# Kernel optimization log

Hardware: AMD Instinct MI355X
Metric: run time of the kernel (lower is better)

Reference implementation:

```python
import jax, jax.numpy as jnp
import numpy as np

N = 500_000      # nodes
B = 8192         # graphs
F = 128          # num_node_features
C = 128          # channels (num_out_features)
EPS = 1e-16      # matches torch_geometric.utils.softmax denominator eps


def setup_inputs() -> dict:
    key = jax.random.key(0)
    ks = jax.random.split(key, 16)
    w = lambda k, shape: jax.random.normal(k, shape, dtype=jnp.float32) * 0.02
    inp = {
        "x": jax.random.normal(ks[0], (N, F), dtype=jnp.float32),
        "u": jax.random.normal(ks[1], (B, C), dtype=jnp.float32),
        "batch": jnp.sort(jax.random.randint(ks[2], (N,), 0, B, dtype=jnp.int32)),
        "size": B,
        # gate_nn: Linear(C,C) -> ReLU -> Linear(C,1)
        "gate_w1": w(ks[3], (C, C)), "gate_b1": w(ks[4], (C,)),
        "gate_w2": w(ks[5], (C, 1)), "gate_b2": w(ks[6], (1,)),
        # node_nn: Linear(F,C) -> ReLU -> Linear(C,C)
        "node_w1": w(ks[7], (F, C)), "node_b1": w(ks[8], (C,)),
        "node_w2": w(ks[9], (C, C)), "node_b2": w(ks[10], (C,)),
        # ques_nn: Linear(C,C) -> ReLU -> Linear(C,C)
        "ques_w1": w(ks[11], (C, C)), "ques_b1": w(ks[12], (C,)),
        "ques_w2": w(ks[13], (C, C)), "ques_b2": w(ks[14], (C,)),
    }
    return inp


def _mlp2(x, w1, b1, w2, b2):
    return jax.nn.relu(x @ w1 + b1) @ w2 + b2


def reference(x, u, batch, size,
              gate_w1, gate_b1, gate_w2, gate_b2,
              node_w1, node_b1, node_w2, node_b2,
              ques_w1, ques_b1, ques_w2, ques_b2):
    # node features h_theta(x): [N, C]
    h = _mlp2(x, node_w1, node_b1, node_w2, node_b2)
    # question features per graph, gathered to nodes: [N, C]
    q = _mlp2(u, ques_w1, ques_b1, ques_w2, ques_b2)
    # gate scores: [N, 1]
    gate = _mlp2(q[batch] * h, gate_w1, gate_b1, gate_w2, gate_b2)
    # segment softmax over graphs (torch_geometric.utils.softmax)
    m = jax.ops.segment_max(gate, batch, num_segments=size)          # [B, 1]
    m = jnp.where(jnp.isfinite(m), m, 0.0)                            # empty segments
    e = jnp.exp(gate - m[batch])                                      # [N, 1]
    s = jax.ops.segment_sum(e, batch, num_segments=size)              # [B, 1]
    alpha = e / (s[batch] + EPS)                                      # [N, 1]
    # scatter_add pooling: [B, C]
    out = jax.ops.segment_sum(alpha * h, batch, num_segments=size)
    return out
```

## Files before the change

### kernel.cpp

```cpp
#include <hip/hip_runtime.h>
#include <math.h>

#define NN 500000
#define NB 8192
#define GMAX 16
#define HG_GRID 1536
#define HG_NT ((NN + 63) / 64)

typedef _Float16 f16x8 __attribute__((ext_vector_type(8)));
typedef __fp16 fp16x2 __attribute__((ext_vector_type(2)));
typedef float f32x4 __attribute__((ext_vector_type(4)));

__device__ inline f16x8 cvt8(float4 a, float4 b) {
    union { fp16x2 p[4]; f16x8 r; } u;
    u.p[0] = __builtin_amdgcn_cvt_pkrtz(a.x, a.y);
    u.p[1] = __builtin_amdgcn_cvt_pkrtz(a.z, a.w);
    u.p[2] = __builtin_amdgcn_cvt_pkrtz(b.x, b.y);
    u.p[3] = __builtin_amdgcn_cvt_pkrtz(b.z, b.w);
    return u.r;
}

__global__ void prep_w(const float* __restrict__ nw1, const float* __restrict__ nw2,
                       const float* __restrict__ gw1, const float* __restrict__ gw2,
                       const float* __restrict__ qw1, const float* __restrict__ qw2,
                       _Float16* __restrict__ wT1, _Float16* __restrict__ wT2,
                       _Float16* __restrict__ wTg, _Float16* __restrict__ wTq1,
                       _Float16* __restrict__ wTq2, _Float16* __restrict__ g2h) {
    int k = blockIdx.x;
    int n = threadIdx.x;
    wT1[n * 128 + k]  = (_Float16)nw1[k * 128 + n];
    wT2[n * 128 + k]  = (_Float16)nw2[k * 128 + n];
    wTg[n * 128 + k]  = (_Float16)gw1[k * 128 + n];
    wTq1[n * 128 + k] = (_Float16)qw1[k * 128 + n];
    wTq2[n * 128 + k] = (_Float16)qw2[k * 128 + n];
    if (k == 0) g2h[n] = (_Float16)gw2[n];
}

__launch_bounds__(512, 4)
__global__ void q_kernel(const float* __restrict__ u,
                         const _Float16* __restrict__ wTq1, const _Float16* __restrict__ wTq2,
                         const float* __restrict__ qb1, const float* __restrict__ qb2,
                         _Float16* __restrict__ q, float* __restrict__ Ppre, float* __restrict__ s) {
    __shared__ __align__(16) _Float16 tbuf[128][136];
    const int tid  = threadIdx.x;
    const int wave = tid >> 6;
    const int lane = tid & 63;
    const int lrow = lane & 15;
    const int quad = lane >> 4;
    const int wr   = wave >> 1;
    const int wc   = wave & 1;
    const int row0 = blockIdx.x * 128;
    const int rbase = wr * 32;

    for (int idx = tid; idx < 128 * 128; idx += 512) Ppre[(size_t)row0 * 128 + idx] = 0.f;
    if (tid < 128) s[row0 + tid] = 0.f;

    f32x4 acc[2][4];
    const f32x4 fz = {0.f, 0.f, 0.f, 0.f};
#pragma unroll
    for (int mi = 0; mi < 2; ++mi)
#pragma unroll
        for (int ci = 0; ci < 4; ++ci) acc[mi][ci] = fz;

#pragma unroll
    for (int ki = 0; ki < 4; ++ki) {
        const int k = ki * 32 + quad * 8;
        f16x8 a[2];
#pragma unroll
        for (int mi = 0; mi < 2; ++mi) {
            int r = row0 + rbase + mi * 16 + lrow;
            const float4* up = (const float4*)(u + (size_t)r * 128 + k);
            a[mi] = cvt8(up[0], up[1]);
        }
        f16x8 b[4];
#pragma unroll
        for (int ci = 0; ci < 4; ++ci)
            b[ci] = *(const f16x8*)(wTq1 + (size_t)(wc * 64 + ci * 16 + lrow) * 128 + k);
#pragma unroll
        for (int mi = 0; mi < 2; ++mi)
#pragma unroll
            for (int ci = 0; ci < 4; ++ci)
                acc[mi][ci] = __builtin_amdgcn_mfma_f32_16x16x32_f16(a[mi], b[ci], acc[mi][ci], 0, 0, 0);
    }
#pragma unroll
    for (int ci = 0; ci < 4; ++ci) {
        int c = wc * 64 + ci * 16 + lrow;
        float bv = qb1[c];
#pragma unroll
        for (int mi = 0; mi < 2; ++mi)
#pragma unroll
            for (int i = 0; i < 4; ++i) {
                int r = rbase + mi * 16 + quad * 4 + i;
                tbuf[r][c] = (_Float16)fmaxf(acc[mi][ci][i] + bv, 0.f);
            }
    }
    __syncthreads();

#pragma unroll
    for (int mi = 0; mi < 2; ++mi)
#pragma unroll
        for (int ci = 0; ci < 4; ++ci) acc[mi][ci] = fz;
#pragma unroll
    for (int ki = 0; ki < 4; ++ki) {
        const int k = ki * 32 + quad * 8;
        f16x8 a[2];
#pragma unroll
        for (int mi = 0; mi < 2; ++mi)
            a[mi] = *(const f16x8*)&tbuf[rbase + mi * 16 + lrow][k];
        f16x8 b[4];
#pragma unroll
        for (int ci = 0; ci < 4; ++ci)
            b[ci] = *(const f16x8*)(wTq2 + (size_t)(wc * 64 + ci * 16 + lrow) * 128 + k);
#pragma unroll
        for (int mi = 0; mi < 2; ++mi)
#pragma unroll
            for (int ci = 0; ci < 4; ++ci)
                acc[mi][ci] = __builtin_amdgcn_mfma_f32_16x16x32_f16(a[mi], b[ci], acc[mi][ci], 0, 0, 0);
    }
#pragma unroll
    for (int ci = 0; ci < 4; ++ci) {
        int c = wc * 64 + ci * 16 + lrow;
        float bv = qb2[c];
#pragma unroll
        for (int mi = 0; mi < 2; ++mi)
#pragma unroll
            for (int i = 0; i < 4; ++i) {
                int r = row0 + rbase + mi * 16 + quad * 4 + i;
                q[(size_t)r * 128 + c] = (_Float16)(acc[mi][ci][i] + bv);
            }
    }
}

__launch_bounds__(256, 1)
__global__ void hg_kernel(const float* __restrict__ x, const int* __restrict__ batch,
                          const _Float16* __restrict__ qglob,
                          const _Float16* __restrict__ wT1, const _Float16* __restrict__ wT2,
                          const _Float16* __restrict__ wTg, const _Float16* __restrict__ g2h,
                          const float* __restrict__ nb1, const float* __restrict__ nb2,
                          const float* __restrict__ gb1, const float* __restrict__ gb2,
                          float* __restrict__ Ppre, float* __restrict__ s) {
    __shared__ __align__(16) _Float16 t1buf[2][64][136];
    __shared__ __align__(16) _Float16 Ebuf[2][GMAX][136];
    __shared__ __align__(16) _Float16 scratch[64][136];

    const int tid  = threadIdx.x;
    const int wave = tid >> 6;
    const int lane = tid & 63;
    const int lrow = lane & 15;
    const int quad = lane >> 4;
    const int rbase = wave * 16;
    const int blk  = (int)blockIdx.x;
    const f32x4 fz = {0.f, 0.f, 0.f, 0.f};

    f16x8 a16[4];
    {
        int r = min(blk * 64 + rbase + lrow, NN - 1);
        const float4* xp = (const float4*)(x + (size_t)r * 128 + quad * 8);
#pragma unroll
        for (int ki = 0; ki < 4; ++ki)
            a16[ki] = cvt8(xp[ki * 8], xp[ki * 8 + 1]);
    }
    int bv = batch[min(blk * 64 + lane, NN - 1)];

    int pb = 0;
    for (int t = blk; t < HG_NT; t += HG_GRID, pb ^= 1) {
        const int row0  = t * 64;
        const int rown0 = (t + HG_GRID) * 64;

        const int b_lo = __shfl(bv, 0, 64);
        int rel = bv - b_lo;
#pragma unroll
        for (int off = 32; off >= 1; off >>= 1) rel = max(rel, __shfl_xor(rel, off, 64));
        const int gcnt = min(rel + 1, GMAX);
        int gown[4];
#pragma unroll
        for (int i = 0; i < 4; ++i)
            gown[i] = __shfl(bv, rbase + quad * 4 + i, 64) - b_lo;
        int bv_next = batch[min(rown0 + lane, NN - 1)];

        {
            int g  = lane >> 2;
            int rr = (lane & 3) * 4;
            *(float2*)&Ebuf[pb][g][rbase + rr] = make_float2(0.f, 0.f);
        }

        f32x4 acc[8];
#pragma unroll
        for (int ci = 0; ci < 8; ++ci) acc[ci] = fz;
#pragma unroll
        for (int ki = 0; ki < 4; ++ki) {
            const int k = ki * 32 + quad * 8;
            f16x8 b[8];
#pragma unroll
            for (int ci = 0; ci < 8; ++ci)
                b[ci] = *(const f16x8*)(wT1 + (size_t)(ci * 16 + lrow) * 128 + k);
#pragma unroll
            for (int ci = 0; ci < 8; ++ci)
                acc[ci] = __builtin_amdgcn_mfma_f32_16x16x32_f16(a16[ki], b[ci], acc[ci], 0, 0, 0);
        }
#pragma unroll
        for (int ci = 0; ci < 8; ++ci) {
            int c = ci * 16 + lrow;
            float bv1 = nb1[c];
#pragma unroll
            for (int i = 0; i < 4; ++i)
                t1buf[pb][rbase + quad * 4 + i][c] = (_Float16)fmaxf(acc[ci][i] + bv1, 0.f);
        }

        __builtin_amdgcn_sched_barrier(0);
        float4 xraw[4][2];
        {
            int r = min(rown0 + rbase + lrow, NN - 1);
            const float4* xp = (const float4*)(x + (size_t)r * 128 + quad * 8);
#pragma unroll
            for (int ki = 0; ki < 4; ++ki) {
                xraw[ki][0] = xp[ki * 8];
                xraw[ki][1] = xp[ki * 8 + 1];
            }
        }

#pragma unroll
        for (int ci = 0; ci < 8; ++ci) acc[ci] = fz;
#pragma unroll
        for (int ki = 0; ki < 4; ++ki) {
            const int k = ki * 32 + quad * 8;
            f16x8 a = *(const f16x8*)&t1buf[pb][rbase + lrow][k];
            f16x8 b[8];
#pragma unroll
            for (int ci = 0; ci < 8; ++ci)
                b[ci] = *(const f16x8*)(wT2 + (size_t)(ci * 16 + lrow) * 128 + k);
#pragma unroll
            for (int ci = 0; ci < 8; ++ci)
                acc[ci] = __builtin_amdgcn_mfma_f32_16x16x32_f16(a, b[ci], acc[ci], 0, 0, 0);
        }
        {
            float nb2c[8];
#pragma unroll
            for (int ci = 0; ci < 8; ++ci) nb2c[ci] = nb2[ci * 16 + lrow];
#pragma unroll
            for (int i = 0; i < 4; ++i) {
                const _Float16* qrow = qglob + (size_t)(b_lo + gown[i]) * 128;
                int r = rbase + quad * 4 + i;
#pragma unroll
                for (int ci = 0; ci < 8; ++ci) {
                    int c = ci * 16 + lrow;
                    float h = acc[ci][i] + nb2c[ci];
                    scratch[r][c] = (_Float16)((float)qrow[c] * h);
                }
            }
        }

#pragma unroll
        for (int ci = 0; ci < 8; ++ci) acc[ci] = fz;
#pragma unroll
        for (int ki = 0; ki < 4; ++ki) {
            const int k = ki * 32 + quad * 8;
            f16x8 a = *(const f16x8*)&scratch[rbase + lrow][k];
            f16x8 b[8];
#pragma unroll
            for (int ci = 0; ci < 8; ++ci)
                b[ci] = *(const f16x8*)(wTg + (size_t)(ci * 16 + lrow) * 128 + k);
#pragma unroll
            for (int ci = 0; ci < 8; ++ci)
                acc[ci] = __builtin_amdgcn_mfma_f32_16x16x32_f16(a, b[ci], acc[ci], 0, 0, 0);
        }
        {
            float p[4] = {0.f, 0.f, 0.f, 0.f};
#pragma unroll
            for (int ci = 0; ci < 8; ++ci) {
                int c = ci * 16 + lrow;
                float b1 = gb1[c];
                float w = (float)g2h[c];
#pragma unroll
                for (int i = 0; i < 4; ++i)
                    p[i] = fmaf(fmaxf(acc[ci][i] + b1, 0.f), w, p[i]);
            }
#pragma unroll
            for (int off = 1; off <= 8; off <<= 1)
#pragma unroll
                for (int i = 0; i < 4; ++i)
                    p[i] += __shfl_xor(p[i], off, 64);
            const float gb2v = gb2[0];
            if (lrow == 0) {
#pragma unroll
                for (int i = 0; i < 4; ++i) {
                    int r = rbase + quad * 4 + i;
                    bool valid = (row0 + r) < NN;
                    float e = valid ? __expf(p[i] + gb2v) : 0.f;
                    int g = gown[i];
                    if (g < GMAX) {
                        Ebuf[pb][g][r] = (_Float16)e;
                    } else if (valid) {
                        atomicAdd(&s[b_lo + g], e);
                        for (int c = 0; c < 128; ++c)
                            atomicAdd(&Ppre[(size_t)(b_lo + g) * 128 + c],
                                      e * (float)t1buf[pb][r][c]);
                    }
                }
            }
        }

#pragma unroll
        for (int ki = 0; ki < 4; ++ki)
            a16[ki] = cvt8(xraw[ki][0], xraw[ki][1]);
        bv = bv_next;

        __syncthreads();

        f16x8 aE[2];
#pragma unroll
        for (int ki2 = 0; ki2 < 2; ++ki2)
            aE[ki2] = *(const f16x8*)&Ebuf[pb][lrow][ki2 * 32 + quad * 8];
        f32x4 pacc[2] = {fz, fz};
#pragma unroll
        for (int ci2 = 0; ci2 < 2; ++ci2) {
            int col = wave * 32 + ci2 * 16 + lrow;
#pragma unroll
            for (int ki2 = 0; ki2 < 2; ++ki2) {
                f16x8 bh;
#pragma unroll
                for (int j = 0; j < 8; ++j) bh[j] = t1buf[pb][ki2 * 32 + quad * 8 + j][col];
                pacc[ci2] = __builtin_amdgcn_mfma_f32_16x16x32_f16(aE[ki2], bh, pacc[ci2], 0, 0, 0);
            }
        }
#pragma unroll
        for (int ci2 = 0; ci2 < 2; ++ci2)
#pragma unroll
            for (int i = 0; i < 4; ++i) {
                int g = quad * 4 + i;
                if (g < gcnt)
                    atomicAdd(&Ppre[(size_t)(b_lo + g) * 128 + wave * 32 + ci2 * 16 + lrow],
                              pacc[ci2][i]);
            }
        if (wave == 0) {
            float sv = 0.f;
#pragma unroll
            for (int j = 0; j < 16; ++j) sv += (float)Ebuf[pb][lrow][quad * 16 + j];
            sv += __shfl_xor(sv, 16, 64);
            sv += __shfl_xor(sv, 32, 64);
            if (quad == 0 && lrow < gcnt) atomicAdd(&s[b_lo + lrow], sv);
        }
    }
}

__launch_bounds__(512, 4)
__global__ void fin_kernel(const float* __restrict__ Ppre, const float* __restrict__ s,
                           const _Float16* __restrict__ wT2, const float* __restrict__ nb2,
                           float* __restrict__ out) {
    const int tid  = threadIdx.x;
    const int wave = tid >> 6;
    const int lane = tid & 63;
    const int lrow = lane & 15;
    const int quad = lane >> 4;
    const int wr   = wave >> 1;
    const int wc   = wave & 1;
    const int row0 = blockIdx.x * 128;
    const int rbase = wr * 32;

    f32x4 acc[2][4];
    const f32x4 fz = {0.f, 0.f, 0.f, 0.f};
#pragma unroll
    for (int mi = 0; mi < 2; ++mi)
#pragma unroll
        for (int ci = 0; ci < 4; ++ci) acc[mi][ci] = fz;
#pragma unroll
    for (int ki = 0; ki < 4; ++ki) {
        const int k = ki * 32 + quad * 8;
        f16x8 a[2];
#pragma unroll
        for (int mi = 0; mi < 2; ++mi) {
            int r = row0 + rbase + mi * 16 + lrow;
            const float4* pp = (const float4*)(Ppre + (size_t)r * 128 + k);
            a[mi] = cvt8(pp[0], pp[1]);
        }
        f16x8 b[4];
#pragma unroll
        for (int ci = 0; ci < 4; ++ci)
            b[ci] = *(const f16x8*)(wT2 + (size_t)(wc * 64 + ci * 16 + lrow) * 128 + k);
#pragma unroll
        for (int mi = 0; mi < 2; ++mi)
#pragma unroll
            for (int ci = 0; ci < 4; ++ci)
                acc[mi][ci] = __builtin_amdgcn_mfma_f32_16x16x32_f16(a[mi], b[ci], acc[mi][ci], 0, 0, 0);
    }
    float sv[2][4], rinv[2][4];
#pragma unroll
    for (int mi = 0; mi < 2; ++mi)
#pragma unroll
        for (int i = 0; i < 4; ++i) {
            int r = row0 + rbase + mi * 16 + quad * 4 + i;
            sv[mi][i] = s[r];
            rinv[mi][i] = 1.f / (sv[mi][i] + 1e-16f);
        }
#pragma unroll
    for (int ci = 0; ci < 4; ++ci) {
        int c = wc * 64 + ci * 16 + lrow;
        float bv = nb2[c];
#pragma unroll
        for (int mi = 0; mi < 2; ++mi)
#pragma unroll
            for (int i = 0; i < 4; ++i) {
                int r = row0 + rbase + mi * 16 + quad * 4 + i;
                out[(size_t)r * 128 + c] = (acc[mi][ci][i] + sv[mi][i] * bv) * rinv[mi][i];
            }
    }
}

extern "C" void kernel_launch(void* const* d_in, const int* in_sizes, int n_in,
                              void* d_out, int out_size, void* d_ws, size_t ws_size,
                              hipStream_t stream) {
    const float* x    = (const float*)d_in[0];
    const float* u    = (const float*)d_in[1];
    const int* batch  = (const int*)d_in[2];
    const float* gw1  = (const float*)d_in[4];
    const float* gb1  = (const float*)d_in[5];
    const float* gw2  = (const float*)d_in[6];
    const float* gb2  = (const float*)d_in[7];
    const float* nw1  = (const float*)d_in[8];
    const float* nb1  = (const float*)d_in[9];
    const float* nw2  = (const float*)d_in[10];
    const float* nb2  = (const float*)d_in[11];
    const float* qw1  = (const float*)d_in[12];
    const float* qb1  = (const float*)d_in[13];
    const float* qw2  = (const float*)d_in[14];
    const float* qb2  = (const float*)d_in[15];

    char* ws = (char*)d_ws;
    _Float16* q   = (_Float16*)ws;
    float* Ppre   = (float*)(ws + 2097152);
    float* s      = (float*)(ws + 6291456);
    _Float16* wT1 = (_Float16*)(ws + 6324224);
    _Float16* wT2  = wT1 + 16384;
    _Float16* wTg  = wT2 + 16384;
    _Float16* wTq1 = wTg + 16384;
    _Float16* wTq2 = wTq1 + 16384;
    _Float16* g2h  = wTq2 + 16384;
    float* out = (float*)d_out;

    hipLaunchKernelGGL(prep_w, dim3(128), dim3(128), 0, stream,
                       nw1, nw2, gw1, gw2, qw1, qw2, wT1, wT2, wTg, wTq1, wTq2, g2h);
    hipLaunchKernelGGL(q_kernel, dim3(NB / 128), dim3(512), 0, stream,
                       u, wTq1, wTq2, qb1, qb2, q, Ppre, s);
    hipLaunchKernelGGL(hg_kernel, dim3(HG_GRID), dim3(256), 0, stream,
                       x, batch, q, wT1, wT2, wTg, g2h, nb1, nb2, gb1, gb2, Ppre, s);
    hipLaunchKernelGGL(fin_kernel, dim3(NB / 128), dim3(512), 0, stream,
                       Ppre, s, wT2, nb2, out);
}
```

Baseline: 598.4 us.

## Double hg_kernel row tile to 128 per block and split next-tile x prefetch

Result: faster. 563.3 us (-5.9%).

```diff
diff --git a/kernel.cpp b/kernel.cpp
--- a/kernel.cpp
+++ b/kernel.cpp
@@ -4,8 +4,9 @@
 #define NN 500000
 #define NB 8192
 #define GMAX 16
-#define HG_GRID 1536
-#define HG_NT ((NN + 63) / 64)
+#define TROWS 128
+#define HG_GRID 512
+#define HG_NT ((NN + TROWS - 1) / TROWS)
 
 typedef _Float16 f16x8 __attribute__((ext_vector_type(8)));
 typedef __fp16 fp16x2 __attribute__((ext_vector_type(2)));
@@ -36,12 +37,12 @@
     if (k == 0) g2h[n] = (_Float16)gw2[n];
 }
 
-__launch_bounds__(512, 4)
+__launch_bounds__(256, 2)
 __global__ void q_kernel(const float* __restrict__ u,
                          const _Float16* __restrict__ wTq1, const _Float16* __restrict__ wTq2,
                          const float* __restrict__ qb1, const float* __restrict__ qb2,
                          _Float16* __restrict__ q, float* __restrict__ Ppre, float* __restrict__ s) {
-    __shared__ __align__(16) _Float16 tbuf[128][136];
+    __shared__ __align__(16) _Float16 tbuf[64][136];
     const int tid  = threadIdx.x;
     const int wave = tid >> 6;
     const int lane = tid & 63;
@@ -49,11 +50,11 @@
     const int quad = lane >> 4;
     const int wr   = wave >> 1;
     const int wc   = wave & 1;
-    const int row0 = blockIdx.x * 128;
+    const int row0 = (int)blockIdx.x * 64;
     const int rbase = wr * 32;
 
-    for (int idx = tid; idx < 128 * 128; idx += 512) Ppre[(size_t)row0 * 128 + idx] = 0.f;
-    if (tid < 128) s[row0 + tid] = 0.f;
+    for (int idx = tid; idx < 64 * 128; idx += 256) Ppre[(size_t)row0 * 128 + idx] = 0.f;
+    if (tid < 64) s[row0 + tid] = 0.f;
 
     f32x4 acc[2][4];
     const f32x4 fz = {0.f, 0.f, 0.f, 0.f};
@@ -139,54 +140,62 @@
                           const float* __restrict__ nb1, const float* __restrict__ nb2,
                           const float* __restrict__ gb1, const float* __restrict__ gb2,
                           float* __restrict__ Ppre, float* __restrict__ s) {
-    __shared__ __align__(16) _Float16 t1buf[2][64][136];
-    __shared__ __align__(16) _Float16 Ebuf[2][GMAX][136];
-    __shared__ __align__(16) _Float16 scratch[64][136];
+    __shared__ __align__(16) _Float16 t1buf[TROWS][136];
+    __shared__ __align__(16) _Float16 scratch[TROWS][136];
+    __shared__ __align__(16) _Float16 Ebuf[GMAX][136];
+    __shared__ int batch_t[TROWS];
 
     const int tid  = threadIdx.x;
     const int wave = tid >> 6;
     const int lane = tid & 63;
     const int lrow = lane & 15;
     const int quad = lane >> 4;
-    const int rbase = wave * 16;
+    const int rbase = wave * 32;
     const int blk  = (int)blockIdx.x;
     const f32x4 fz = {0.f, 0.f, 0.f, 0.f};
 
-    f16x8 a16[4];
+    f16x8 a16[4][2];
     {
-        int r = min(blk * 64 + rbase + lrow, NN - 1);
-        const float4* xp = (const float4*)(x + (size_t)r * 128 + quad * 8);
+        const int r0 = blk * TROWS;
 #pragma unroll
         for (int ki = 0; ki < 4; ++ki)
-            a16[ki] = cvt8(xp[ki * 8], xp[ki * 8 + 1]);
-    }
-    int bv = batch[min(blk * 64 + lane, NN - 1)];
-
-    int pb = 0;
-    for (int t = blk; t < HG_NT; t += HG_GRID, pb ^= 1) {
-        const int row0  = t * 64;
-        const int rown0 = (t + HG_GRID) * 64;
-
-        const int b_lo = __shfl(bv, 0, 64);
-        int rel = bv - b_lo;
-#pragma unroll
-        for (int off = 32; off >= 1; off >>= 1) rel = max(rel, __shfl_xor(rel, off, 64));
-        const int gcnt = min(rel + 1, GMAX);
-        int gown[4];
-#pragma unroll
-        for (int i = 0; i < 4; ++i)
-            gown[i] = __shfl(bv, rbase + quad * 4 + i, 64) - b_lo;
-        int bv_next = batch[min(rown0 + lane, NN - 1)];
+#pragma unroll
+            for (int mi = 0; mi < 2; ++mi) {
+                int r = min(r0 + rbase + mi * 16 + lrow, NN - 1);
+                const float4* xp = (const float4*)(x + (size_t)r * 128 + ki * 32 + quad * 8);
+                a16[ki][mi] = cvt8(xp[0], xp[1]);
+            }
+    }
+    int bvr = batch[min(blk * TROWS + rbase + (lane & 31), NN - 1)];
+
+    for (int t = blk; t < HG_NT; t += HG_GRID) {
+        const int row0  = t * TROWS;
+        const int rown0 = (t + HG_GRID) * TROWS;
+
+        if (lane < 32) batch_t[rbase + lane] = bvr;
+        __syncthreads();
+        const int b_lo = batch_t[0];
+        const int gcnt = min(batch_t[TROWS - 1] - b_lo + 1, GMAX);
+        bvr = batch[min(rown0 + rbase + (lane & 31), NN - 1)];
+
+        int gown[2][4];
+#pragma unroll
+        for (int mi = 0; mi < 2; ++mi)
+#pragma unroll
+            for (int i = 0; i < 4; ++i)
+                gown[mi][i] = batch_t[rbase + mi * 16 + quad * 4 + i] - b_lo;
 
         {
-            int g  = lane >> 2;
-            int rr = (lane & 3) * 4;
-            *(float2*)&Ebuf[pb][g][rbase + rr] = make_float2(0.f, 0.f);
-        }
-
-        f32x4 acc[8];
-#pragma unroll
-        for (int ci = 0; ci < 8; ++ci) acc[ci] = fz;
+            int g = lane >> 2;
+            int r0e = rbase + (lane & 3) * 8;
+            *(float4*)&Ebuf[g][r0e] = make_float4(0.f, 0.f, 0.f, 0.f);
+        }
+
+        f32x4 acc[2][8];
+#pragma unroll
+        for (int mi = 0; mi < 2; ++mi)
+#pragma unroll
+            for (int ci = 0; ci < 8; ++ci) acc[mi][ci] = fz;
 #pragma unroll
         for (int ki = 0; ki < 4; ++ki) {
             const int k = ki * 32 + quad * 8;
@@ -195,131 +204,165 @@
             for (int ci = 0; ci < 8; ++ci)
                 b[ci] = *(const f16x8*)(wT1 + (size_t)(ci * 16 + lrow) * 128 + k);
 #pragma unroll
-            for (int ci = 0; ci < 8; ++ci)
-                acc[ci] = __builtin_amdgcn_mfma_f32_16x16x32_f16(a16[ki], b[ci], acc[ci], 0, 0, 0);
+            for (int mi = 0; mi < 2; ++mi)
+#pragma unroll
+                for (int ci = 0; ci < 8; ++ci)
+                    acc[mi][ci] = __builtin_amdgcn_mfma_f32_16x16x32_f16(a16[ki][mi], b[ci], acc[mi][ci], 0, 0, 0);
         }
 #pragma unroll
         for (int ci = 0; ci < 8; ++ci) {
             int c = ci * 16 + lrow;
             float bv1 = nb1[c];
 #pragma unroll
-            for (int i = 0; i < 4; ++i)
-                t1buf[pb][rbase + quad * 4 + i][c] = (_Float16)fmaxf(acc[ci][i] + bv1, 0.f);
+            for (int mi = 0; mi < 2; ++mi)
+#pragma unroll
+                for (int i = 0; i < 4; ++i)
+                    t1buf[rbase + mi * 16 + quad * 4 + i][c] = (_Float16)fmaxf(acc[mi][ci][i] + bv1, 0.f);
         }
 
         __builtin_amdgcn_sched_barrier(0);
-        float4 xraw[4][2];
-        {
-            int r = min(rown0 + rbase + lrow, NN - 1);
-            const float4* xp = (const float4*)(x + (size_t)r * 128 + quad * 8);
-#pragma unroll
-            for (int ki = 0; ki < 4; ++ki) {
-                xraw[ki][0] = xp[ki * 8];
-                xraw[ki][1] = xp[ki * 8 + 1];
-            }
-        }
-
-#pragma unroll
-        for (int ci = 0; ci < 8; ++ci) acc[ci] = fz;
+        float4 xrawA[2][2][2];
+#pragma unroll
+        for (int ki = 0; ki < 2; ++ki)
+#pragma unroll
+            for (int mi = 0; mi < 2; ++mi) {
+                int r = min(rown0 + rbase + mi * 16 + lrow, NN - 1);
+                const float4* xp = (const float4*)(x + (size_t)r * 128 + ki * 32 + quad * 8);
+                xrawA[ki][mi][0] = xp[0];
+                xrawA[ki][mi][1] = xp[1];
+            }
+
+#pragma unroll
+        for (int mi = 0; mi < 2; ++mi)
+#pragma unroll
+            for (int ci = 0; ci < 8; ++ci) acc[mi][ci] = fz;
 #pragma unroll
         for (int ki = 0; ki < 4; ++ki) {
             const int k = ki * 32 + quad * 8;
-            f16x8 a = *(const f16x8*)&t1buf[pb][rbase + lrow][k];
+            f16x8 a[2];
+#pragma unroll
+            for (int mi = 0; mi < 2; ++mi)
+                a[mi] = *(const f16x8*)&t1buf[rbase + mi * 16 + lrow][k];
             f16x8 b[8];
 #pragma unroll
             for (int ci = 0; ci < 8; ++ci)
                 b[ci] = *(const f16x8*)(wT2 + (size_t)(ci * 16 + lrow) * 128 + k);
 #pragma unroll
-            for (int ci = 0; ci < 8; ++ci)
-                acc[ci] = __builtin_amdgcn_mfma_f32_16x16x32_f16(a, b[ci], acc[ci], 0, 0, 0);
-        }
-        {
-            float nb2c[8];
-#pragma unroll
-            for (int ci = 0; ci < 8; ++ci) nb2c[ci] = nb2[ci * 16 + lrow];
+            for (int mi = 0; mi < 2; ++mi)
+#pragma unroll
+                for (int ci = 0; ci < 8; ++ci)
+                    acc[mi][ci] = __builtin_amdgcn_mfma_f32_16x16x32_f16(a[mi], b[ci], acc[mi][ci], 0, 0, 0);
+        }
+#pragma unroll
+        for (int mi = 0; mi < 2; ++mi)
 #pragma unroll
             for (int i = 0; i < 4; ++i) {
-                const _Float16* qrow = qglob + (size_t)(b_lo + gown[i]) * 128;
-                int r = rbase + quad * 4 + i;
+                int r = rbase + mi * 16 + quad * 4 + i;
+                const _Float16* qrow = qglob + (size_t)(b_lo + gown[mi][i]) * 128;
 #pragma unroll
                 for (int ci = 0; ci < 8; ++ci) {
                     int c = ci * 16 + lrow;
-                    float h = acc[ci][i] + nb2c[ci];
+                    float h = acc[mi][ci][i] + nb2[c];
                     scratch[r][c] = (_Float16)((float)qrow[c] * h);
                 }
             }
-        }
-
-#pragma unroll
-        for (int ci = 0; ci < 8; ++ci) acc[ci] = fz;
+
+#pragma unroll
+        for (int ki = 0; ki < 2; ++ki)
+#pragma unroll
+            for (int mi = 0; mi < 2; ++mi)
+                a16[ki][mi] = cvt8(xrawA[ki][mi][0], xrawA[ki][mi][1]);
+
+#pragma unroll
+        for (int mi = 0; mi < 2; ++mi)
+#pragma unroll
+            for (int ci = 0; ci < 8; ++ci) acc[mi][ci] = fz;
 #pragma unroll
         for (int ki = 0; ki < 4; ++ki) {
             const int k = ki * 32 + quad * 8;
-            f16x8 a = *(const f16x8*)&scratch[rbase + lrow][k];
+            f16x8 a[2];
+#pragma unroll
+            for (int mi = 0; mi < 2; ++mi)
+                a[mi] = *(const f16x8*)&scratch[rbase + mi * 16 + lrow][k];
             f16x8 b[8];
 #pragma unroll
             for (int ci = 0; ci < 8; ++ci)
                 b[ci] = *(const f16x8*)(wTg + (size_t)(ci * 16 + lrow) * 128 + k);
 #pragma unroll
-            for (int ci = 0; ci < 8; ++ci)
-                acc[ci] = __builtin_amdgcn_mfma_f32_16x16x32_f16(a, b[ci], acc[ci], 0, 0, 0);
-        }
+            for (int mi = 0; mi < 2; ++mi)
+#pragma unroll
+                for (int ci = 0; ci < 8; ++ci)
+                    acc[mi][ci] = __builtin_amdgcn_mfma_f32_16x16x32_f16(a[mi], b[ci], acc[mi][ci], 0, 0, 0);
+        }
+
+        __builtin_amdgcn_sched_barrier(0);
+        float4 xrawB[2][2][2];
+#pragma unroll
+        for (int ki = 0; ki < 2; ++ki)
+#pragma unroll
+            for (int mi = 0; mi < 2; ++mi) {
+                int r = min(rown0 + rbase + mi * 16 + lrow, NN - 1);
+                const float4* xp = (const float4*)(x + (size_t)r * 128 + (ki + 2) * 32 + quad * 8);
+                xrawB[ki][mi][0] = xp[0];
+                xrawB[ki][mi][1] = xp[1];
+            }
+
         {
-            float p[4] = {0.f, 0.f, 0.f, 0.f};
+            float p[2][4] = {{0.f, 0.f, 0.f, 0.f}, {0.f, 0.f, 0.f, 0.f}};
 #pragma unroll
             for (int ci = 0; ci < 8; ++ci) {
                 int c = ci * 16 + lrow;
                 float b1 = gb1[c];
                 float w = (float)g2h[c];
 #pragma unroll
-                for (int i = 0; i < 4; ++i)
-                    p[i] = fmaf(fmaxf(acc[ci][i] + b1, 0.f), w, p[i]);
+                for (int mi = 0; mi < 2; ++mi)
+#pragma unroll
+                    for (int i = 0; i < 4; ++i)
+                        p[mi][i] = fmaf(fmaxf(acc[mi][ci][i] + b1, 0.f), w, p[mi][i]);
             }
 #pragma unroll
             for (int off = 1; off <= 8; off <<= 1)
 #pragma unroll
-                for (int i = 0; i < 4; ++i)
-                    p[i] += __shfl_xor(p[i], off, 64);
+                for (int mi = 0; mi < 2; ++mi)
+#pragma unroll
+                    for (int i = 0; i < 4; ++i)
+                        p[mi][i] += __shfl_xor(p[mi][i], off, 64);
             const float gb2v = gb2[0];
             if (lrow == 0) {
 #pragma unroll
-                for (int i = 0; i < 4; ++i) {
-                    int r = rbase + quad * 4 + i;
-                    bool valid = (row0 + r) < NN;
-                    float e = valid ? __expf(p[i] + gb2v) : 0.f;
-                    int g = gown[i];
-                    if (g < GMAX) {
-                        Ebuf[pb][g][r] = (_Float16)e;
-                    } else if (valid) {
-                        atomicAdd(&s[b_lo + g], e);
-                        for (int c = 0; c < 128; ++c)
-                            atomicAdd(&Ppre[(size_t)(b_lo + g) * 128 + c],
-                                      e * (float)t1buf[pb][r][c]);
+                for (int mi = 0; mi < 2; ++mi)
+#pragma unroll
+                    for (int i = 0; i < 4; ++i) {
+                        int r = rbase + mi * 16 + quad * 4 + i;
+                        bool valid = (row0 + r) < NN;
+                        float e = valid ? __expf(p[mi][i] + gb2v) : 0.f;
+                        int g = gown[mi][i];
+                        if (g < GMAX) {
+                            Ebuf[g][r] = (_Float16)e;
+                        } else if (valid) {
+                            atomicAdd(&s[b_lo + g], e);
+                            for (int c = 0; c < 128; ++c)
+                                atomicAdd(&Ppre[(size_t)(b_lo + g) * 128 + c],
+                                          e * (float)t1buf[r][c]);
+                        }
                     }
-                }
-            }
-        }
-
-#pragma unroll
-        for (int ki = 0; ki < 4; ++ki)
-            a16[ki] = cvt8(xraw[ki][0], xraw[ki][1]);
-        bv = bv_next;
-
+            }
+        }
         __syncthreads();
 
-        f16x8 aE[2];
-#pragma unroll
-        for (int ki2 = 0; ki2 < 2; ++ki2)
-            aE[ki2] = *(const f16x8*)&Ebuf[pb][lrow][ki2 * 32 + quad * 8];
+        f16x8 aE[4];
+#pragma unroll
+        for (int ki2 = 0; ki2 < 4; ++ki2)
+            aE[ki2] = *(const f16x8*)&Ebuf[lrow][ki2 * 32 + quad * 8];
         f32x4 pacc[2] = {fz, fz};
 #pragma unroll
         for (int ci2 = 0; ci2 < 2; ++ci2) {
             int col = wave * 32 + ci2 * 16 + lrow;
 #pragma unroll
-            for (int ki2 = 0; ki2 < 2; ++ki2) {
+            for (int ki2 = 0; ki2 < 4; ++ki2) {
                 f16x8 bh;
 #pragma unroll
-                for (int j = 0; j < 8; ++j) bh[j] = t1buf[pb][ki2 * 32 + quad * 8 + j][col];
+                for (int j = 0; j < 8; ++j) bh[j] = t1buf[ki2 * 32 + quad * 8 + j][col];
                 pacc[ci2] = __builtin_amdgcn_mfma_f32_16x16x32_f16(aE[ki2], bh, pacc[ci2], 0, 0, 0);
             }
         }
@@ -335,15 +378,21 @@
         if (wave == 0) {
             float sv = 0.f;
 #pragma unroll
-            for (int j = 0; j < 16; ++j) sv += (float)Ebuf[pb][lrow][quad * 16 + j];
+            for (int j = 0; j < 32; ++j) sv += (float)Ebuf[lrow][quad * 32 + j];
             sv += __shfl_xor(sv, 16, 64);
             sv += __shfl_xor(sv, 32, 64);
             if (quad == 0 && lrow < gcnt) atomicAdd(&s[b_lo + lrow], sv);
         }
-    }
-}
-
-__launch_bounds__(512, 4)
+
+#pragma unroll
+        for (int ki = 0; ki < 2; ++ki)
+#pragma unroll
+            for (int mi = 0; mi < 2; ++mi)
+                a16[ki + 2][mi] = cvt8(xrawB[ki][mi][0], xrawB[ki][mi][1]);
+    }
+}
+
+__launch_bounds__(256, 2)
 __global__ void fin_kernel(const float* __restrict__ Ppre, const float* __restrict__ s,
                            const _Float16* __restrict__ wT2, const float* __restrict__ nb2,
                            float* __restrict__ out) {
@@ -354,55 +403,43 @@
     const int quad = lane >> 4;
     const int wr   = wave >> 1;
     const int wc   = wave & 1;
-    const int row0 = blockIdx.x * 128;
-    const int rbase = wr * 32;
-
-    f32x4 acc[2][4];
+    const int row0 = (int)blockIdx.x * 32;
+    const int rbase = wr * 16;
+
+    f32x4 acc[4];
     const f32x4 fz = {0.f, 0.f, 0.f, 0.f};
 #pragma unroll
-    for (int mi = 0; mi < 2; ++mi)
-#pragma unroll
-        for (int ci = 0; ci < 4; ++ci) acc[mi][ci] = fz;
+    for (int ci = 0; ci < 4; ++ci) acc[ci] = fz;
 #pragma unroll
     for (int ki = 0; ki < 4; ++ki) {
         const int k = ki * 32 + quad * 8;
-        f16x8 a[2];
-#pragma unroll
-        for (int mi = 0; mi < 2; ++mi) {
-            int r = row0 + rbase + mi * 16 + lrow;
-            const float4* pp = (const float4*)(Ppre + (size_t)r * 128 + k);
-            a[mi] = cvt8(pp[0], pp[1]);
-        }
+        int r = row0 + rbase + lrow;
+        const float4* pp = (const float4*)(Ppre + (size_t)r * 128 + k);
+        f16x8 a = cvt8(pp[0], pp[1]);
         f16x8 b[4];
 #pragma unroll
         for (int ci = 0; ci < 4; ++ci)
             b[ci] = *(const f16x8*)(wT2 + (size_t)(wc * 64 + ci * 16 + lrow) * 128 + k);
 #pragma unroll
-        for (int mi = 0; mi < 2; ++mi)
-#pragma unroll
-            for (int ci = 0; ci < 4; ++ci)
-                acc[mi][ci] = __builtin_amdgcn_mfma_f32_16x16x32_f16(a[mi], b[ci], acc[mi][ci], 0, 0, 0);
-    }
-    float sv[2][4], rinv[2][4];
-#pragma unroll
-    for (int mi = 0; mi < 2; ++mi)
-#pragma unroll
-        for (int i = 0; i < 4; ++i) {
-            int r = row0 + rbase + mi * 16 + quad * 4 + i;
-            sv[mi][i] = s[r];
-            rinv[mi][i] = 1.f / (sv[mi][i] + 1e-16f);
-        }
+        for (int ci = 0; ci < 4; ++ci)
+            acc[ci] = __builtin_amdgcn_mfma_f32_16x16x32_f16(a, b[ci], acc[ci], 0, 0, 0);
+    }
+    float sv[4], rinv[4];
+#pragma unroll
+    for (int i = 0; i < 4; ++i) {
+        int r = row0 + rbase + quad * 4 + i;
+        sv[i] = s[r];
+        rinv[i] = 1.f / (sv[i] + 1e-16f);
+    }
 #pragma unroll
     for (int ci = 0; ci < 4; ++ci) {
         int c = wc * 64 + ci * 16 + lrow;
         float bv = nb2[c];
 #pragma unroll
-        for (int mi = 0; mi < 2; ++mi)
-#pragma unroll
-            for (int i = 0; i < 4; ++i) {
-                int r = row0 + rbase + mi * 16 + quad * 4 + i;
-                out[(size_t)r * 128 + c] = (acc[mi][ci][i] + sv[mi][i] * bv) * rinv[mi][i];
-            }
+        for (int i = 0; i < 4; ++i) {
+            int r = row0 + rbase + quad * 4 + i;
+            out[(size_t)r * 128 + c] = (acc[ci][i] + sv[i] * bv) * rinv[i];
+        }
     }
 }
 
@@ -439,10 +476,10 @@
 
     hipLaunchKernelGGL(prep_w, dim3(128), dim3(128), 0, stream,
                        nw1, nw2, gw1, gw2, qw1, qw2, wT1, wT2, wTg, wTq1, wTq2, g2h);
-    hipLaunchKernelGGL(q_kernel, dim3(NB / 128), dim3(512), 0, stream,
+    hipLaunchKernelGGL(q_kernel, dim3(NB / 64), dim3(256), 0, stream,
                        u, wTq1, wTq2, qb1, qb2, q, Ppre, s);
     hipLaunchKernelGGL(hg_kernel, dim3(HG_GRID), dim3(256), 0, stream,
                        x, batch, q, wT1, wT2, wTg, g2h, nb1, nb2, gb1, gb2, Ppre, s);
-    hipLaunchKernelGGL(fin_kernel, dim3(NB / 128), dim3(512), 0, stream,
+    hipLaunchKernelGGL(fin_kernel, dim3(NB / 32), dim3(256), 0, stream,
                        Ppre, s, wT2, nb2, out);
 }
```
